# Optimization experiments

Hardware: AMD Instinct MI355X
Metric: run time of the kernel (lower is better)

Reference implementation:

```python
import jax, jax.numpy as jnp
import numpy as np

N = 100_000      # nodes
E = 1_600_000    # edges
G = 512          # graphs in batch
C_IN, H, C_OUT = 128, 128, 10
MU = 1.0
MAX_ITER = 10
BN_EPS = 1e-5


def setup_inputs() -> dict:
    key = jax.random.key(0)
    ks = jax.random.split(key, 24)
    inp = {}
    inp['x'] = jax.random.normal(ks[0], (N, C_IN), dtype=jnp.float32)
    inp['edge_index'] = jax.random.randint(ks[1], (2, E), 0, N, dtype=jnp.int64)
    inp['edge_weight'] = jax.random.uniform(ks[2], (E,), dtype=jnp.float32)
    inp['batch'] = jnp.sort(jax.random.randint(ks[3], (N,), 0, G, dtype=jnp.int64))
    s = lambda k, shp: jax.random.normal(k, shp, dtype=jnp.float32) * 0.05
    # MLP: in -> 64 -> H -> H
    inp['mlp_w1'] = s(ks[4], (C_IN, 64)); inp['mlp_b1'] = jnp.zeros((64,), jnp.float32)
    inp['mlp_w2'] = s(ks[5], (64, H));    inp['mlp_b2'] = jnp.zeros((H,), jnp.float32)
    inp['mlp_w3'] = s(ks[6], (H, H));     inp['mlp_b3'] = jnp.zeros((H,), jnp.float32)
    # BatchNorm1d (eval mode: running stats)
    inp['bn_gamma'] = jnp.ones((H,), jnp.float32)
    inp['bn_beta'] = jnp.zeros((H,), jnp.float32)
    inp['bn_mean'] = s(ks[7], (H,))
    inp['bn_var'] = jax.random.uniform(ks[8], (H,), dtype=jnp.float32) + 0.5
    # node-level FC stack (num_layers=2) and graph-level FC stack
    inp['fc_w'] = s(ks[9], (2, H, H));  inp['fc_b'] = jnp.zeros((2, H), jnp.float32)
    inp['gfc_w'] = s(ks[10], (2, H, H)); inp['gfc_b'] = jnp.zeros((2, H), jnp.float32)
    inp['final_w'] = s(ks[11], (H, C_OUT)); inp['final_b'] = jnp.zeros((C_OUT,), jnp.float32)
    return inp


def reference(x, edge_weight, mlp_w1, mlp_b1, mlp_w2, mlp_b2, mlp_w3, mlp_b3,
              bn_gamma, bn_beta, bn_mean, bn_var, fc_w, fc_b, gfc_w, gfc_b,
              final_w, final_b, edge_index, batch):
    row, col = edge_index[0], edge_index[1]
    # random-walk normalization D^{-1} A (weighted out-degree at destination row)
    deg = jax.ops.segment_sum(edge_weight, row, num_segments=N)
    deg_inv = 1.0 / jnp.clip(deg, 1e-12, None)

    # MLP encoder (dropout = identity in eval mode)
    h = jax.nn.relu(x @ mlp_w1 + mlp_b1)
    h = jax.nn.relu(h @ mlp_w2 + mlp_b2)
    h = h @ mlp_w3 + mlp_b3
    # BatchNorm1d, eval mode
    h = (h - bn_mean) * jax.lax.rsqrt(bn_var + BN_EPS) * bn_gamma + bn_beta

    # DEQ fixed-point: z = (D^-1 A z + mu * h) / (1 + mu), fixed MAX_ITER iterations
    def step(z, _):
        msg = edge_weight[:, None] * z[col]            # [E, H]
        agg = jax.ops.segment_sum(msg, row, num_segments=N)
        z_new = (agg * deg_inv[:, None] + MU * h) / (1.0 + MU)
        return z_new, None

    z0 = jnp.zeros_like(h)
    z, _ = jax.lax.scan(step, z0, None, length=MAX_ITER)

    # node FC stack
    for i in range(2):
        z = jax.nn.relu(z @ fc_w[i] + fc_b[i])
    # global_add_pool over graphs
    g = jax.ops.segment_sum(z, batch, num_segments=G)   # [G, H]
    # graph FC stack
    for i in range(2):
        g = jax.nn.relu(g @ gfc_w[i] + gfc_b[i])
    out = g @ final_w + final_b
    return jax.nn.log_softmax(out, axis=1)
```

## Files before the change

### kernel.cpp

```cpp
#include <hip/hip_runtime.h>

#define NN 100000
#define NE 1600000
#define NG 512
#define HD 128
#define NBUK 782
#define EPAD 1903104

typedef short short8 __attribute__((ext_vector_type(8)));
typedef float f32x4 __attribute__((ext_vector_type(4)));
typedef uint uintx4 __attribute__((ext_vector_type(4)));

__device__ __forceinline__ ushort f2b(float v) {
    uint u = __float_as_uint(v);
    u = (u + 0x7fffu + ((u >> 16) & 1u)) >> 16;
    return (ushort)u;
}
__device__ __forceinline__ uint pkbf(float a, float b) {
    return (uint)f2b(a) | ((uint)f2b(b) << 16);
}
__device__ __forceinline__ float blo(uint u) { return __uint_as_float(u << 16); }
__device__ __forceinline__ float bhi(uint u) { return __uint_as_float(u & 0xffff0000u); }

__global__ void detect_kernel(const unsigned* __restrict__ ei, int* __restrict__ flag) {
    unsigned v = ei[threadIdx.x * 2 + 1];
    unsigned long long m = __ballot(v != 0u);
    if (threadIdx.x == 0) flag[0] = (m == 0ull) ? 1 : 0;
}

__device__ __forceinline__ int load_idx(const void* p, long long i, int is64) {
    return is64 ? (int)((const long long*)p)[i] : ((const int*)p)[i];
}

__global__ __launch_bounds__(256) void bkt_count(const void* __restrict__ eiv, const int* __restrict__ flag,
                                                 int* __restrict__ bcnt, int E) {
    __shared__ int h[NBUK];
    for (int i = threadIdx.x; i < NBUK; i += 256) h[i] = 0;
    __syncthreads();
    int is64 = *flag;
    int stride = gridDim.x * 256;
    for (int i = blockIdx.x * 256 + threadIdx.x; i < E; i += stride) {
        int r = load_idx(eiv, i, is64);
        atomicAdd(&h[r >> 7], 1);
    }
    __syncthreads();
    for (int i = threadIdx.x; i < NBUK; i += 256) {
        int v = h[i];
        if (v) atomicAdd(&bcnt[i], v);
    }
}

__global__ __launch_bounds__(1024) void bucket_scan(const int* __restrict__ bcnt, int* __restrict__ bstart,
                                                    int* __restrict__ bcur) {
    __shared__ int s[1024];
    int t = threadIdx.x;
    int own = (t < NBUK) ? (((bcnt[t] + 3) & ~3) + 384) : 0;
    s[t] = own;
    __syncthreads();
    for (int off = 1; off < 1024; off <<= 1) {
        int v = (t >= off) ? s[t - off] : 0;
        __syncthreads();
        s[t] += v;
        __syncthreads();
    }
    if (t < NBUK) {
        int excl = s[t] - own;
        bstart[t] = excl;
        bcur[t] = excl;
    }
    if (t == NBUK - 1) bstart[NBUK] = s[t];
}

__global__ __launch_bounds__(256) void bkt_scatter(const void* __restrict__ eiv, const float* __restrict__ ew,
                                                   const int* __restrict__ flag, int* __restrict__ bcur,
                                                   unsigned char* __restrict__ brow, int2* __restrict__ bcw, int E) {
    __shared__ int h[NBUK];
    __shared__ int c[NBUK];
    for (int i = threadIdx.x; i < NBUK; i += 256) { h[i] = 0; c[i] = 0; }
    __syncthreads();
    int is64 = *flag;
    int per = (E + gridDim.x - 1) / gridDim.x;
    int e0 = blockIdx.x * per, e1 = min(e0 + per, E);
    for (int i = e0 + threadIdx.x; i < e1; i += 256) {
        int r = load_idx(eiv, i, is64);
        atomicAdd(&h[r >> 7], 1);
    }
    __syncthreads();
    for (int i = threadIdx.x; i < NBUK; i += 256) {
        int v = h[i];
        h[i] = v ? atomicAdd(&bcur[i], v) : 0;
    }
    __syncthreads();
    for (int i = e0 + threadIdx.x; i < e1; i += 256) {
        int r = load_idx(eiv, i, is64);
        int col = load_idx(eiv, (long long)E + i, is64);
        int b = r >> 7;
        int pos = h[b] + atomicAdd(&c[b], 1);
        brow[pos] = (unsigned char)(r & 127);
        bcw[pos] = make_int2(col, __float_as_int(ew[i]));
    }
}

__global__ __launch_bounds__(256) void bkt_finalize(const int* __restrict__ bstart, const int* __restrict__ bcnt,
                                                    const unsigned char* __restrict__ brow,
                                                    const int2* __restrict__ bcw, int* __restrict__ rowptr,
                                                    uint* __restrict__ edges4, float* __restrict__ dscale) {
    __shared__ int rh[128];
    __shared__ int prb[128];
    __shared__ int rc[128];
    __shared__ float wsum[128];
    int b = blockIdx.x;
    int t = threadIdx.x;
    if (t < 128) { rh[t] = 0; rc[t] = 0; wsum[t] = 0.f; }
    __syncthreads();
    int s0 = bstart[b];
    int s1r = s0 + bcnt[b];
    for (int j = s0 + t; j < s1r; j += 256) atomicAdd(&rh[brow[j]], 1);
    __syncthreads();
    if (t < 128) prb[t] = (rh[t] + 3) & ~3;
    __syncthreads();
    for (int off = 1; off < 128; off <<= 1) {
        int v = 0;
        if (t < 128 && t >= off) v = prb[t - off];
        __syncthreads();
        if (t < 128) prb[t] += v;
        __syncthreads();
    }
    int rows = min(128, NN - b * 128);
    if (t < rows) rowptr[b * 128 + t] = s0 + prb[t] - ((rh[t] + 3) & ~3);
    if (b == NBUK - 1 && t == rows - 1) rowptr[NN] = s0 + prb[t];
    __syncthreads();
    for (int j = s0 + t; j < s1r; j += 256) {
        int2 cw = bcw[j];
        int r = brow[j];
        int pos = s0 + prb[r] - ((rh[r] + 3) & ~3) + atomicAdd(&rc[r], 1);
        float w = __int_as_float(cw.y);
        edges4[pos] = ((uint)cw.x << 15) | (uint)(f2b(w) & 0x7fff);
        atomicAdd(&wsum[r], w);
    }
    __syncthreads();
    if (t < rows) {
        dscale[b * 128 + t] = 0.5f / fmaxf(wsum[t], 1e-12f);
        int start = s0 + prb[t] - ((rh[t] + 3) & ~3);
        int cnt = rh[t], pc = (cnt + 3) & ~3;
        for (int j = cnt; j < pc; j++) edges4[start + j] = 0;
    }
}

__global__ void wprep(const float* __restrict__ W, ushort* __restrict__ Wt, int K, int OC) {
    int c = blockIdx.x;
    int k = threadIdx.x;
    if (k >= K) return;
    int g = k >> 3, j = k & 7;
    Wt[c * K + (((g ^ (c & 7)) << 3) | j)] = f2b(W[k * OC + c]);
}

template <int K, int OC, int EPI, bool AF32>
__global__ __launch_bounds__(256) void mgemm(const void* __restrict__ A, const ushort* __restrict__ Wt,
                                             const float* __restrict__ bias, ushort* __restrict__ C, int nrows,
                                             const float* __restrict__ bng, const float* __restrict__ bnb,
                                             const float* __restrict__ bnm, const float* __restrict__ bnv,
                                             unsigned char* __restrict__ hpf8) {
    constexpr int GPR = K / 8;
    __shared__ __align__(16) char smem[64 * K * 2 + OC * K * 2];
    char* Al = smem;
    char* Wl = smem + 64 * K * 2;

    const int t = threadIdx.x;
    const int rowbase = blockIdx.x * 64;

#pragma unroll
    for (int ch = t; ch < 64 * GPR; ch += 256) {
        int row = ch / GPR, g = ch % GPR;
        int gn = rowbase + row;
        uint4 w = make_uint4(0, 0, 0, 0);
        if (gn < nrows) {
            if (AF32) {
                const float4* p = (const float4*)((const float*)A + (size_t)gn * K + g * 8);
                float4 a0 = p[0], a1 = p[1];
                w.x = pkbf(a0.x, a0.y); w.y = pkbf(a0.z, a0.w);
                w.z = pkbf(a1.x, a1.y); w.w = pkbf(a1.z, a1.w);
            } else {
                w = *(const uint4*)((const ushort*)A + (size_t)gn * K + g * 8);
            }
        }
        *(uint4*)(Al + row * (2 * K) + ((g ^ (row & 7)) << 4)) = w;
    }
#pragma unroll
    for (int ch = t; ch < OC * GPR; ch += 256) {
        ((uint4*)Wl)[ch] = ((const uint4*)Wt)[ch];
    }
    __syncthreads();

    const int l = t & 63, wv = t >> 6;
    const int lrow = wv * 16 + (l & 15);
    const int lg = l >> 4;

    f32x4 acc[OC / 16];
#pragma unroll
    for (int i = 0; i < OC / 16; i++) acc[i] = (f32x4){0.f, 0.f, 0.f, 0.f};

#pragma unroll
    for (int kk = 0; kk < K / 32; kk++) {
        int ga = kk * 4 + lg;
        short8 af = *(const short8*)(Al + lrow * (2 * K) + ((ga ^ (lrow & 7)) << 4));
#pragma unroll
        for (int ct = 0; ct < OC / 16; ct++) {
            int c = ct * 16 + (l & 15);
            short8 bfr = *(const short8*)(Wl + c * (2 * K) + ((ga ^ (c & 7)) << 4));
            acc[ct] = __builtin_amdgcn_mfma_f32_16x16x32_bf16(af, bfr, acc[ct], 0, 0, 0);
        }
    }

#pragma unroll
    for (int ct = 0; ct < OC / 16; ct++) {
        int c = ct * 16 + (l & 15);
        float bia = bias[c];
        float scale = 0.f, shift = 0.f;
        if (EPI == 1) {
            float rs = rsqrtf(bnv[c] + 1e-5f) * bng[c];
            scale = 0.5f * rs;
            shift = 0.5f * (bnb[c] - bnm[c] * rs);
        }
#pragma unroll
        for (int r = 0; r < 4; r++) {
            int gn = rowbase + wv * 16 + (l >> 4) * 4 + r;
            if (gn < nrows) {
                float v = acc[ct][r] + bia;
                if (EPI == 0) {
                    v = fmaxf(v, 0.f);
                    C[(size_t)gn * OC + c] = f2b(v);
                } else {
                    v = v * scale + shift;
                    C[(size_t)gn * OC + c] = f2b(v);
                    int pk8 = __builtin_amdgcn_cvt_pk_fp8_f32(v, v, 0, false);
                    hpf8[(size_t)gn * OC + c] = (unsigned char)(pk8 & 0xff);
                }
            }
        }
    }
}

__device__ __forceinline__ void acc16(const uintx4 zv, float w, float* a) {
#pragma unroll
    for (int wi = 0; wi < 4; wi++) {
        uint word = zv[wi];
        auto lo = __builtin_amdgcn_cvt_pk_f32_fp8((int)word, false);
        auto hi = __builtin_amdgcn_cvt_pk_f32_fp8((int)word, true);
        a[wi * 4 + 0] += w * lo[0];
        a[wi * 4 + 1] += w * lo[1];
        a[wi * 4 + 2] += w * hi[0];
        a[wi * 4 + 3] += w * hi[1];
    }
}
#define GATH16(c) (*(const uintx4*)(zin + ((size_t)((c) >> 15) << 7) + (lq << 4)))
#define WOF(x) __uint_as_float(((x) & 0x7fffu) << 16)

template <int OUTF>
__global__ __launch_bounds__(256) void deq_step(const unsigned char* __restrict__ zin, void* __restrict__ zout,
                                                const unsigned char* __restrict__ hpb, const float* __restrict__ dscale,
                                                const int* __restrict__ rowptr, const uint* __restrict__ edges) {
    const int t = threadIdx.x;
    const int n = blockIdx.x * 32 + (t >> 3);
    const int lq = t & 7;
    const int s = rowptr[n], e = rowptr[n + 1];
    float a[16];
#pragma unroll
    for (int i = 0; i < 16; i++) a[i] = 0.f;

    if (s < e) {
        uintx4 erA = *(const uintx4*)(edges + s);
        uintx4 zA0 = GATH16(erA.x), zA1 = GATH16(erA.y), zA2 = GATH16(erA.z), zA3 = GATH16(erA.w);
        uintx4 erB = erA;
        if (s + 4 < e) erB = *(const uintx4*)(edges + s + 4);
        for (int i = s + 4; i < e; i += 4) {
            uintx4 erC = erB;
            if (i + 4 < e) erC = *(const uintx4*)(edges + i + 4);
            uintx4 zB0 = GATH16(erB.x), zB1 = GATH16(erB.y), zB2 = GATH16(erB.z), zB3 = GATH16(erB.w);
            acc16(zA0, WOF(erA.x), a);
            acc16(zA1, WOF(erA.y), a);
            acc16(zA2, WOF(erA.z), a);
            acc16(zA3, WOF(erA.w), a);
            erA = erB;
            zA0 = zB0; zA1 = zB1; zA2 = zB2; zA3 = zB3;
            erB = erC;
        }
        acc16(zA0, WOF(erA.x), a);
        acc16(zA1, WOF(erA.y), a);
        acc16(zA2, WOF(erA.z), a);
        acc16(zA3, WOF(erA.w), a);
    }

    float ds = dscale[n];
    const uintx4 hb0 = *(const uintx4*)(hpb + ((size_t)n << 8) + (lq << 5));
    const uintx4 hb1 = *(const uintx4*)(hpb + ((size_t)n << 8) + (lq << 5) + 16);
    float o[16];
#pragma unroll
    for (int k = 0; k < 8; k++) {
        uint h = (k < 4) ? hb0[k] : hb1[k - 4];
        o[2 * k] = a[2 * k] * ds + blo(h);
        o[2 * k + 1] = a[2 * k + 1] * ds + bhi(h);
    }

    if (OUTF == 1) {
        uintx4 u;
#pragma unroll
        for (int wi = 0; wi < 4; wi++) {
            int pk = __builtin_amdgcn_cvt_pk_fp8_f32(o[wi * 4], o[wi * 4 + 1], 0, false);
            pk = __builtin_amdgcn_cvt_pk_fp8_f32(o[wi * 4 + 2], o[wi * 4 + 3], pk, true);
            u[wi] = (uint)pk;
        }
        uintx4* dst = (uintx4*)((unsigned char*)zout + ((size_t)n << 7) + (lq << 4));
        *dst = u;
    } else {
        uintx4 u0, u1;
#pragma unroll
        for (int k = 0; k < 4; k++) u0[k] = pkbf(o[2 * k], o[2 * k + 1]);
#pragma unroll
        for (int k = 0; k < 4; k++) u1[k] = pkbf(o[8 + 2 * k], o[8 + 2 * k + 1]);
        unsigned char* base = (unsigned char*)zout + ((size_t)n << 8) + (lq << 5);
        __builtin_nontemporal_store(u0, (uintx4*)base);
        __builtin_nontemporal_store(u1, (uintx4*)(base + 16));
    }
}

__global__ __launch_bounds__(64) void pool_kernel(const uint* __restrict__ z, const void* __restrict__ batchv,
                                                  const int* __restrict__ flag, float* __restrict__ gpool, int n) {
    const int l = threadIdx.x;
    int n0 = blockIdx.x * 64;
    int n1 = min(n0 + 64, n);
    int is64 = *flag;
    float rx = 0.f, ry = 0.f;
    int cur = -1;
    for (int i = n0; i < n1; i++) {
        int b = load_idx(batchv, i, is64);
        if (b != cur) {
            if (cur >= 0) {
                atomicAdd(&gpool[cur * HD + 2 * l], rx);
                atomicAdd(&gpool[cur * HD + 2 * l + 1], ry);
            }
            rx = 0.f; ry = 0.f;
            cur = b;
        }
        uint zb = z[(size_t)i * 64 + l];
        rx += blo(zb);
        ry += bhi(zb);
    }
    if (cur >= 0) {
        atomicAdd(&gpool[cur * HD + 2 * l], rx);
        atomicAdd(&gpool[cur * HD + 2 * l + 1], ry);
    }
}

__global__ __launch_bounds__(128) void graph_kernel(const float* __restrict__ gpool, const float* __restrict__ gfc_w,
                                                    const float* __restrict__ gfc_b, const float* __restrict__ fw,
                                                    const float* __restrict__ fb, float* __restrict__ out) {
    __shared__ float buf[HD];
    __shared__ float o[10];
    __shared__ float ls;
    const int g = blockIdx.x, t = threadIdx.x;
    buf[t] = gpool[g * HD + t];
    __syncthreads();
    for (int L = 0; L < 2; L++) {
        const float* w = gfc_w + L * HD * HD;
        float s = gfc_b[L * HD + t];
        for (int k = 0; k < HD; k++) s += buf[k] * w[k * HD + t];
        s = fmaxf(s, 0.f);
        __syncthreads();
        buf[t] = s;
        __syncthreads();
    }
    if (t < 10) {
        float s = fb[t];
        for (int k = 0; k < HD; k++) s += buf[k] * fw[k * 10 + t];
        o[t] = s;
    }
    __syncthreads();
    if (t == 0) {
        float m = o[0];
        for (int i = 1; i < 10; i++) m = fmaxf(m, o[i]);
        float se = 0.f;
        for (int i = 0; i < 10; i++) se += expf(o[i] - m);
        ls = m + logf(se);
    }
    __syncthreads();
    if (t < 10) out[g * 10 + t] = o[t] - ls;
}

extern "C" void kernel_launch(void* const* d_in, const int* in_sizes, int n_in,
                              void* d_out, int out_size, void* d_ws, size_t ws_size,
                              hipStream_t stream) {
    const float* x = (const float*)d_in[0];
    const void* eiv = d_in[1];
    const float* ew = (const float*)d_in[2];
    const void* batchv = d_in[3];
    const float* mlp_w1 = (const float*)d_in[4];
    const float* mlp_b1 = (const float*)d_in[5];
    const float* mlp_w2 = (const float*)d_in[6];
    const float* mlp_b2 = (const float*)d_in[7];
    const float* mlp_w3 = (const float*)d_in[8];
    const float* mlp_b3 = (const float*)d_in[9];
    const float* bn_g = (const float*)d_in[10];
    const float* bn_b = (const float*)d_in[11];
    const float* bn_m = (const float*)d_in[12];
    const float* bn_v = (const float*)d_in[13];
    const float* fc_w = (const float*)d_in[14];
    const float* fc_b = (const float*)d_in[15];
    const float* gfc_w = (const float*)d_in[16];
    const float* gfc_b = (const float*)d_in[17];
    const float* fin_w = (const float*)d_in[18];
    const float* fin_b = (const float*)d_in[19];
    float* out = (float*)d_out;

    char* ws = (char*)d_ws;
    size_t off = 0;
    auto alloc = [&](size_t bytes) -> void* {
        void* p = ws + off;
        off = (off + bytes + 255) & ~(size_t)255;
        return p;
    };
    ushort* hpb = (ushort*)alloc((size_t)NN * HD * 2);
    unsigned char* hpf8 = (unsigned char*)alloc((size_t)NN * HD);
    ushort* za = (ushort*)alloc((size_t)NN * HD * 2);
    unsigned char* zf8a = (unsigned char*)alloc((size_t)NN * HD);
    unsigned char* zf8b = (unsigned char*)alloc((size_t)NN * HD);
    uint* edges4 = (uint*)alloc((size_t)EPAD * 4);
    ushort* bfA = (ushort*)alloc((size_t)NN * HD * 2);
    char* region2 = (char*)alloc((size_t)NN * HD * 2);
    unsigned char* brow = (unsigned char*)region2;
    int2* bcw = (int2*)(region2 + (size_t)EPAD);
    ushort* bfB = (ushort*)region2;
    int* rowptr = (int*)alloc((size_t)(NN + 1) * 4);
    float* dscale = (float*)alloc((size_t)NN * 4);
    int* bcnt = (int*)alloc((size_t)NBUK * 4);
    int* bstart = (int*)alloc((size_t)(NBUK + 1) * 4);
    int* bcur = (int*)alloc((size_t)NBUK * 4);
    float* gpool = (float*)alloc((size_t)NG * HD * 4);
    int* flag = (int*)alloc(256);
    ushort* w1t = (ushort*)alloc(128 * 64 * 2);
    ushort* w2t = (ushort*)alloc(64 * 128 * 2);
    ushort* w3t = (ushort*)alloc(128 * 128 * 2);
    ushort* f1t = (ushort*)alloc(128 * 128 * 2);
    ushort* f2t = (ushort*)alloc(128 * 128 * 2);

    hipMemsetAsync(bcnt, 0, (size_t)NBUK * 4, stream);
    hipMemsetAsync(gpool, 0, (size_t)NG * HD * 4, stream);

    detect_kernel<<<1, 64, 0, stream>>>((const unsigned*)eiv, flag);
    bkt_count<<<256, 256, 0, stream>>>(eiv, flag, bcnt, NE);
    bucket_scan<<<1, 1024, 0, stream>>>(bcnt, bstart, bcur);
    bkt_scatter<<<256, 256, 0, stream>>>(eiv, ew, flag, bcur, brow, bcw, NE);
    bkt_finalize<<<NBUK, 256, 0, stream>>>(bstart, bcnt, brow, bcw, rowptr, edges4, dscale);

    wprep<<<64, 128, 0, stream>>>(mlp_w1, w1t, 128, 64);
    wprep<<<128, 64, 0, stream>>>(mlp_w2, w2t, 64, 128);
    wprep<<<128, 128, 0, stream>>>(mlp_w3, w3t, 128, 128);
    wprep<<<128, 128, 0, stream>>>(fc_w, f1t, 128, 128);
    wprep<<<128, 128, 0, stream>>>(fc_w + 128 * 128, f2t, 128, 128);

    const int GB = (NN + 63) / 64;
    mgemm<128, 64, 0, true><<<GB, 256, 0, stream>>>(x, w1t, mlp_b1, bfA, NN, nullptr, nullptr, nullptr, nullptr, nullptr);
    mgemm<64, 128, 0, false><<<GB, 256, 0, stream>>>(bfA, w2t, mlp_b2, bfB, NN, nullptr, nullptr, nullptr, nullptr, nullptr);
    mgemm<128, 128, 1, false><<<GB, 256, 0, stream>>>(bfB, w3t, mlp_b3, hpb, NN, bn_g, bn_b, bn_m, bn_v, hpf8);

    const int DB = (NN + 31) / 32;
    deq_step<1><<<DB, 256, 0, stream>>>(hpf8, zf8a, (const unsigned char*)hpb, dscale, rowptr, edges4);
    {
        unsigned char* bufs[2] = {zf8a, zf8b};
        for (int it = 1; it < 8; it++) {
            deq_step<1><<<DB, 256, 0, stream>>>(bufs[(it + 1) & 1], bufs[it & 1], (const unsigned char*)hpb,
                                                dscale, rowptr, edges4);
        }
    }
    deq_step<0><<<DB, 256, 0, stream>>>(zf8b, za, (const unsigned char*)hpb, dscale, rowptr, edges4);

    mgemm<128, 128, 0, false><<<GB, 256, 0, stream>>>(za, f1t, fc_b, bfA, NN, nullptr, nullptr, nullptr, nullptr, nullptr);
    mgemm<128, 128, 0, false><<<GB, 256, 0, stream>>>(bfA, f2t, fc_b + 128, bfB, NN, nullptr, nullptr, nullptr, nullptr, nullptr);

    pool_kernel<<<(NN + 63) / 64, 64, 0, stream>>>((const uint*)bfB, batchv, flag, gpool, NN);
    graph_kernel<<<NG, 128, 0, stream>>>(gpool, gfc_w, gfc_b, fin_w, fin_b, out);
}
```

Before: 859.3 us.

## Split each node's edge list across two waves and reduce via LDS

Each DEQ step now assigns two wavefronts per group of 8 nodes, each taking alternating 4-edge chunks, and combines the partial sums through shared memory before the epilogue. This doubles memory-level parallelism for the edge gather and halves per-thread serial latency on high-degree rows. The fp8 iterations also read the fp8 copy of h instead of the bf16 one, which halves that read but adds fp8 quantisation error to the h term. The cost is a block-wide barrier, LDS traffic, and half the threads idling in the epilogue.

```diff
diff --git a/kernel.cpp b/kernel.cpp
--- a/kernel.cpp
+++ b/kernel.cpp
@@ -258,24 +258,30 @@
 
 template <int OUTF>
 __global__ __launch_bounds__(256) void deq_step(const unsigned char* __restrict__ zin, void* __restrict__ zout,
-                                                const unsigned char* __restrict__ hpb, const float* __restrict__ dscale,
+                                                const unsigned char* __restrict__ hpany, const float* __restrict__ dscale,
                                                 const int* __restrict__ rowptr, const uint* __restrict__ edges) {
+    __shared__ float lds[16 * 8 * 16];
     const int t = threadIdx.x;
-    const int n = blockIdx.x * 32 + (t >> 3);
-    const int lq = t & 7;
+    const int wid = t >> 6;
+    const int wk = wid & 1;
+    const int lane = t & 63;
+    const int g = lane >> 3, lq = lane & 7;
+    const int nl = (wid >> 1) * 8 + g;
+    const int n = blockIdx.x * 16 + nl;
     const int s = rowptr[n], e = rowptr[n + 1];
     float a[16];
 #pragma unroll
     for (int i = 0; i < 16; i++) a[i] = 0.f;
 
-    if (s < e) {
-        uintx4 erA = *(const uintx4*)(edges + s);
+    int i0 = s + wk * 4;
+    if (i0 < e) {
+        uintx4 erA = *(const uintx4*)(edges + i0);
         uintx4 zA0 = GATH16(erA.x), zA1 = GATH16(erA.y), zA2 = GATH16(erA.z), zA3 = GATH16(erA.w);
         uintx4 erB = erA;
-        if (s + 4 < e) erB = *(const uintx4*)(edges + s + 4);
-        for (int i = s + 4; i < e; i += 4) {
+        if (i0 + 8 < e) erB = *(const uintx4*)(edges + i0 + 8);
+        for (int i = i0 + 8; i < e; i += 8) {
             uintx4 erC = erB;
-            if (i + 4 < e) erC = *(const uintx4*)(edges + i + 4);
+            if (i + 8 < e) erC = *(const uintx4*)(edges + i + 8);
             uintx4 zB0 = GATH16(erB.x), zB1 = GATH16(erB.y), zB2 = GATH16(erB.z), zB3 = GATH16(erB.w);
             acc16(zA0, WOF(erA.x), a);
             acc16(zA1, WOF(erA.y), a);
@@ -291,18 +297,32 @@
         acc16(zA3, WOF(erA.w), a);
     }
 
+    if (wk == 1) {
+        float* dst = &lds[(nl * 8 + lq) * 16];
+#pragma unroll
+        for (int j = 0; j < 16; j++) dst[j] = a[j];
+    }
+    __syncthreads();
+    if (wk == 1) return;
+    {
+        const float* src = &lds[(nl * 8 + lq) * 16];
+#pragma unroll
+        for (int j = 0; j < 16; j++) a[j] += src[j];
+    }
+
     float ds = dscale[n];
-    const uintx4 hb0 = *(const uintx4*)(hpb + ((size_t)n << 8) + (lq << 5));
-    const uintx4 hb1 = *(const uintx4*)(hpb + ((size_t)n << 8) + (lq << 5) + 16);
     float o[16];
-#pragma unroll
-    for (int k = 0; k < 8; k++) {
-        uint h = (k < 4) ? hb0[k] : hb1[k - 4];
-        o[2 * k] = a[2 * k] * ds + blo(h);
-        o[2 * k + 1] = a[2 * k + 1] * ds + bhi(h);
-    }
-
     if (OUTF == 1) {
+        const uintx4 hz = *(const uintx4*)(hpany + ((size_t)n << 7) + (lq << 4));
+#pragma unroll
+        for (int wi = 0; wi < 4; wi++) {
+            auto lo = __builtin_amdgcn_cvt_pk_f32_fp8((int)hz[wi], false);
+            auto hi = __builtin_amdgcn_cvt_pk_f32_fp8((int)hz[wi], true);
+            o[wi * 4 + 0] = a[wi * 4 + 0] * ds + lo[0];
+            o[wi * 4 + 1] = a[wi * 4 + 1] * ds + lo[1];
+            o[wi * 4 + 2] = a[wi * 4 + 2] * ds + hi[0];
+            o[wi * 4 + 3] = a[wi * 4 + 3] * ds + hi[1];
+        }
         uintx4 u;
 #pragma unroll
         for (int wi = 0; wi < 4; wi++) {
@@ -313,6 +333,14 @@
         uintx4* dst = (uintx4*)((unsigned char*)zout + ((size_t)n << 7) + (lq << 4));
         *dst = u;
     } else {
+        const uintx4 hb0 = *(const uintx4*)(hpany + ((size_t)n << 8) + (lq << 5));
+        const uintx4 hb1 = *(const uintx4*)(hpany + ((size_t)n << 8) + (lq << 5) + 16);
+#pragma unroll
+        for (int k = 0; k < 8; k++) {
+            uint h = (k < 4) ? hb0[k] : hb1[k - 4];
+            o[2 * k] = a[2 * k] * ds + blo(h);
+            o[2 * k + 1] = a[2 * k + 1] * ds + bhi(h);
+        }
         uintx4 u0, u1;
 #pragma unroll
         for (int k = 0; k < 4; k++) u0[k] = pkbf(o[2 * k], o[2 * k + 1]);
@@ -463,12 +491,12 @@
     mgemm<64, 128, 0, false><<<GB, 256, 0, stream>>>(bfA, w2t, mlp_b2, bfB, NN, nullptr, nullptr, nullptr, nullptr, nullptr);
     mgemm<128, 128, 1, false><<<GB, 256, 0, stream>>>(bfB, w3t, mlp_b3, hpb, NN, bn_g, bn_b, bn_m, bn_v, hpf8);
 
-    const int DB = (NN + 31) / 32;
-    deq_step<1><<<DB, 256, 0, stream>>>(hpf8, zf8a, (const unsigned char*)hpb, dscale, rowptr, edges4);
+    const int DB = NN / 16;
+    deq_step<1><<<DB, 256, 0, stream>>>(hpf8, zf8a, hpf8, dscale, rowptr, edges4);
     {
         unsigned char* bufs[2] = {zf8a, zf8b};
         for (int it = 1; it < 8; it++) {
-            deq_step<1><<<DB, 256, 0, stream>>>(bufs[(it + 1) & 1], bufs[it & 1], (const unsigned char*)hpb,
+            deq_step<1><<<DB, 256, 0, stream>>>(bufs[(it + 1) & 1], bufs[it & 1], hpf8,
                                                 dscale, rowptr, edges4);
         }
     }
```

Measured after the change: 1.125 ms. 30.9% more time.
